# Optimization experiments

Hardware: AMD Instinct MI355X
Metric: run time of the kernel (lower is better)

Reference implementation:

```python
import jax, jax.numpy as jnp
import numpy as np

H, W, D = 160, 160, 16
VOXEL_SIZE = 0.4
VOL_MIN = np.array([-32.0, -32.0, -1.0], dtype=np.float32)
SCALE_MULTIPLIER = 3.0
N_GAUSS = 8192
CHUNK = 64


def setup_inputs() -> dict:
    key = jax.random.key(0)
    k1, k2, k3, k4, k5 = jax.random.split(key, 5)
    vol_min = jnp.asarray(VOL_MIN)
    vol_ext = jnp.array([64.0, 64.0, 6.4], dtype=jnp.float32)
    means3d = jax.random.uniform(k1, (N_GAUSS, 3), jnp.float32) * vol_ext + vol_min
    opacities = jax.random.uniform(k2, (N_GAUSS, 1), jnp.float32)
    # per-axis std devs: 0.2..0.8 m so 3-sigma footprint spans a handful of voxels
    scales = 0.2 + 0.6 * jax.random.uniform(k3, (N_GAUSS, 3), jnp.float32)
    rotations = jax.random.normal(k4, (N_GAUSS, 4), jnp.float32)
    features = jax.random.normal(k5, (N_GAUSS, 32), jnp.float32)
    return {"means3d": means3d, "opacities": opacities, "scales": scales,
            "rotations": rotations, "features": features}


def quat_to_rotmat(q):
    # q: [N,4] wxyz, normalized
    w, x, y, z = q[:, 0], q[:, 1], q[:, 2], q[:, 3]
    R = jnp.stack([
        jnp.stack([1 - 2 * (y * y + z * z), 2 * (x * y - w * z), 2 * (x * z + w * y)], -1),
        jnp.stack([2 * (x * y + w * z), 1 - 2 * (x * x + z * z), 2 * (y * z - w * x)], -1),
        jnp.stack([2 * (x * z - w * y), 2 * (y * z + w * x), 1 - 2 * (x * x + y * y)], -1),
    ], axis=-2)  # [N,3,3]
    return R


def _grid_coords():
    ii, jj, kk = jnp.meshgrid(jnp.arange(H), jnp.arange(W), jnp.arange(D), indexing="ij")
    idx = jnp.stack([ii, jj, kk], axis=-1).astype(jnp.float32)
    return (idx + 0.5) * VOXEL_SIZE + jnp.asarray(VOL_MIN)  # [H,W,D,3] voxel centers


def reference(means3d, opacities, scales, rotations, features):
    x = _grid_coords().reshape(-1, 3)  # [V,3]
    q = rotations / jnp.linalg.norm(rotations, axis=-1, keepdims=True)
    R = quat_to_rotmat(q)
    # covariance = R diag(s^2) R^T
    cov = jnp.einsum("nij,nj,nkj->nik", R, scales * scales, R)
    cov_inv = jnp.linalg.inv(cov)
    sigma = jnp.sqrt(jnp.diagonal(cov, axis1=1, axis2=2))  # [N,3]
    opac = opacities[:, 0]  # [N]
    n = means3d.shape[0]
    nchunks = n // CHUNK

    def chunked(a):
        return a.reshape(nchunks, CHUNK, *a.shape[1:])

    def step(acc, c):
        mu, op, sg, ci, ft = c
        diff = x[:, None, :] - mu[None, :, :]  # [V,CHUNK,3]
        maha = jnp.einsum("vci,cij,vcj->vc", diff, ci, diff)
        # local aggregation cutoff: within scale_multiplier * sigma box around mean
        mask = jnp.all(jnp.abs(diff) <= SCALE_MULTIPLIER * sg[None, :, :], axis=-1)
        w = op[None, :] * jnp.exp(-0.5 * maha) * mask  # [V,CHUNK]
        return acc + w @ ft, None

    acc0 = jnp.zeros((x.shape[0], features.shape[-1]), jnp.float32)
    xs = (chunked(means3d), chunked(opac), chunked(sigma), chunked(cov_inv), chunked(features))
    acc, _ = jax.lax.scan(step, acc0, xs)
    return acc.reshape(H, W, D, features.shape[-1])
```

## Files before the change

### kernel.cpp

```cpp
#include <hip/hip_runtime.h>

#define HH 160
#define WW 160
#define DD 16
#define NG 8192
#define VOXEL 0.4f

#define TTX 20
#define TTY 20
#define TTZ 4
#define NTILES (TTX * TTY * TTZ)
#define CAP 256


__global__ __launch_bounds__(64) void gv_precompute_bin(
    const float* __restrict__ means, const float* __restrict__ opac,
    const float* __restrict__ scales, const float* __restrict__ rots,
    float4* __restrict__ pack, int* __restrict__ tileCnt,
    int* __restrict__ tileList) {
  int g = blockIdx.x * 64 + threadIdx.x;
  if (g >= NG) return;
  float qw = rots[g * 4 + 0], qx = rots[g * 4 + 1];
  float qy = rots[g * 4 + 2], qz = rots[g * 4 + 3];
  float inv = rsqrtf(qw * qw + qx * qx + qy * qy + qz * qz);
  qw *= inv; qx *= inv; qy *= inv; qz *= inv;
  float R[3][3];
  R[0][0] = 1.f - 2.f * (qy * qy + qz * qz);
  R[0][1] = 2.f * (qx * qy - qw * qz);
  R[0][2] = 2.f * (qx * qz + qw * qy);
  R[1][0] = 2.f * (qx * qy + qw * qz);
  R[1][1] = 1.f - 2.f * (qx * qx + qz * qz);
  R[1][2] = 2.f * (qy * qz - qw * qx);
  R[2][0] = 2.f * (qx * qz - qw * qy);
  R[2][1] = 2.f * (qy * qz + qw * qx);
  R[2][2] = 1.f - 2.f * (qx * qx + qy * qy);
  float sx = scales[g * 3 + 0], sy = scales[g * 3 + 1], sz = scales[g * 3 + 2];
  float s2[3] = {sx * sx, sy * sy, sz * sz};
  float is2[3] = {1.f / s2[0], 1.f / s2[1], 1.f / s2[2]};
  float cov00 = 0.f, cov11 = 0.f, cov22 = 0.f;
  float ci00 = 0.f, ci01 = 0.f, ci02 = 0.f, ci11 = 0.f, ci12 = 0.f, ci22 = 0.f;
#pragma unroll
  for (int c = 0; c < 3; c++) {
    cov00 += R[0][c] * R[0][c] * s2[c];
    cov11 += R[1][c] * R[1][c] * s2[c];
    cov22 += R[2][c] * R[2][c] * s2[c];
    ci00 += R[0][c] * R[0][c] * is2[c];
    ci01 += R[0][c] * R[1][c] * is2[c];
    ci02 += R[0][c] * R[2][c] * is2[c];
    ci11 += R[1][c] * R[1][c] * is2[c];
    ci12 += R[1][c] * R[2][c] * is2[c];
    ci22 += R[2][c] * R[2][c] * is2[c];
  }
  float mx = means[g * 3 + 0], my = means[g * 3 + 1], mz = means[g * 3 + 2];
  float bx = 3.f * sqrtf(cov00), by = 3.f * sqrtf(cov11), bz = 3.f * sqrtf(cov22);
  float4* p = pack + (size_t)g * 4;
  p[0] = make_float4(mx, my, mz, opac[g]);
  p[1] = make_float4(bx, by, bz, ci00);
  p[2] = make_float4(ci01, ci02, ci11, ci12);
  p[3] = make_float4(ci22, 0.f, 0.f, 0.f);

  const float eps = 1e-4f;
  int i0 = (int)ceilf((mx - bx + 32.f) * 2.5f - 0.5f - eps);
  int i1 = (int)floorf((mx + bx + 32.f) * 2.5f - 0.5f + eps);
  int j0 = (int)ceilf((my - by + 32.f) * 2.5f - 0.5f - eps);
  int j1 = (int)floorf((my + by + 32.f) * 2.5f - 0.5f + eps);
  int k0 = (int)ceilf((mz - bz + 1.f) * 2.5f - 0.5f - eps);
  int k1 = (int)floorf((mz + bz + 1.f) * 2.5f - 0.5f + eps);
  i0 = max(i0, 0); i1 = min(i1, HH - 1);
  j0 = max(j0, 0); j1 = min(j1, WW - 1);
  k0 = max(k0, 0); k1 = min(k1, DD - 1);
  if (i0 > i1 || j0 > j1 || k0 > k1) return;
  int ti0 = i0 >> 3, ti1 = i1 >> 3;
  int tj0 = j0 >> 3, tj1 = j1 >> 3;
  int tk0 = k0 >> 2, tk1 = k1 >> 2;
  for (int ti = ti0; ti <= ti1; ti++)
    for (int tj = tj0; tj <= tj1; tj++)
      for (int tk = tk0; tk <= tk1; tk++) {
        int t = (ti * TTY + tj) * TTZ + tk;
        int pos = atomicAdd(&tileCnt[t], 1);
        if (pos < CAP) tileList[t * CAP + pos] = g;
      }
}

__global__ __launch_bounds__(256) void gv_voxelize(
    const float4* __restrict__ pack, const float4* __restrict__ feats,
    const int* __restrict__ tileCnt, const int* __restrict__ tileList,
    float4* __restrict__ out) {
  int tid = threadIdx.x;
  int dk = tid & 3, dj = (tid >> 2) & 7, di = tid >> 5;
  int tk = blockIdx.x, tj = blockIdx.y, ti = blockIdx.z;
  int i = ti * 8 + di, j = tj * 8 + dj, k = tk * 4 + dk;

  float px = (i + 0.5f) * VOXEL - 32.f;
  float py = (j + 0.5f) * VOXEL - 32.f;
  float pz = (k + 0.5f) * VOXEL - 1.f;

  int t = (ti * TTY + tj) * TTZ + tk;
  int cnt = min(tileCnt[t], CAP);
  const int* lst = tileList + t * CAP;

  float4 acc[8];
#pragma unroll
  for (int f = 0; f < 8; f++) acc[f] = make_float4(0.f, 0.f, 0.f, 0.f);

#pragma unroll 2
  for (int n = 0; n < cnt; n++) {
    int gg = lst[n];
    const float4* p = pack + (size_t)gg * 4;
    float4 pa = p[0];
    float4 pb = p[1];
    float dx = px - pa.x, dy = py - pa.y, dz = pz - pa.z;
    bool in = (fabsf(dx) <= pb.x) & (fabsf(dy) <= pb.y) & (fabsf(dz) <= pb.z);
    if (__any(in)) {
      float4 pc = p[2];
      float4 pd = p[3];
      float maha = pb.w * dx * dx + pc.z * dy * dy + pd.x * dz * dz +
                   2.f * (pc.x * dx * dy + pc.y * dx * dz + pc.w * dy * dz);
      float w = in ? pa.w * __expf(-0.5f * maha) : 0.f;
      const float4* ft = feats + (size_t)gg * 8;
#pragma unroll
      for (int f = 0; f < 8; f++) {
        float4 fv = ft[f];
        acc[f].x += w * fv.x;
        acc[f].y += w * fv.y;
        acc[f].z += w * fv.z;
        acc[f].w += w * fv.w;
      }
    }
  }

  size_t v = ((size_t)i * WW + j) * DD + k;
  float4* o = out + v * 8;
#pragma unroll
  for (int f = 0; f < 8; f++) o[f] = acc[f];
}

extern "C" void kernel_launch(void* const* d_in, const int* in_sizes, int n_in,
                              void* d_out, int out_size, void* d_ws, size_t ws_size,
                              hipStream_t stream) {
  const float* means  = (const float*)d_in[0];
  const float* opac   = (const float*)d_in[1];
  const float* scales = (const float*)d_in[2];
  const float* rots   = (const float*)d_in[3];
  const float4* feats = (const float4*)d_in[4];

  char* ws = (char*)d_ws;
  float4* pack   = (float4*)ws;
  int* tileCnt   = (int*)(ws + 512 * 1024);
  int* tileList  = (int*)(ws + 520 * 1024);

  hipMemsetAsync(tileCnt, 0, NTILES * sizeof(int), stream);
  gv_precompute_bin<<<NG / 64, 64, 0, stream>>>(means, opac, scales, rots,
                                                pack, tileCnt, tileList);
  dim3 grid(TTZ, TTY, TTX);
  gv_voxelize<<<grid, 256, 0, stream>>>(pack, feats, tileCnt, tileList,
                                        (float4*)d_out);
}
```

Before: 138.2 us.

## Shrink voxel tiles to one wave each and scalarize Gaussian parameter loads

Binning moves from 8x8x4 to 4x4x4 voxel tiles, and each 64-lane wave now owns one tile, so every voxel tests fewer Gaussians that cannot reach it. Each wave loads its tile's index list cooperatively, one index per lane. It then broadcasts each index with shfl plus readfirstlane, which makes the parameter and feature addresses wave-uniform and lets them become scalar loads. The per-Gaussian __any early-out is dropped, and per-tile capacity falls to 128. In exchange there are more binning atomics, a larger tile list, and a risk of silent truncation if a tile ever holds more than 128 Gaussians.

New measurement: 129.4 us. 6.3% less time.

```diff
diff --git a/kernel.cpp b/kernel.cpp
--- a/kernel.cpp
+++ b/kernel.cpp
@@ -6,11 +6,11 @@
 #define NG 8192
 #define VOXEL 0.4f
 
-#define TTX 20
-#define TTY 20
+#define TTX 40
+#define TTY 40
 #define TTZ 4
 #define NTILES (TTX * TTY * TTZ)
-#define CAP 256
+#define CAP 128
 
 
 __global__ __launch_bounds__(64) void gv_precompute_bin(
@@ -70,8 +70,8 @@
   j0 = max(j0, 0); j1 = min(j1, WW - 1);
   k0 = max(k0, 0); k1 = min(k1, DD - 1);
   if (i0 > i1 || j0 > j1 || k0 > k1) return;
-  int ti0 = i0 >> 3, ti1 = i1 >> 3;
-  int tj0 = j0 >> 3, tj1 = j1 >> 3;
+  int ti0 = i0 >> 2, ti1 = i1 >> 2;
+  int tj0 = j0 >> 2, tj1 = j1 >> 2;
   int tk0 = k0 >> 2, tk1 = k1 >> 2;
   for (int ti = ti0; ti <= ti1; ti++)
     for (int tj = tj0; tj <= tj1; tj++)
@@ -82,14 +82,17 @@
       }
 }
 
-__global__ __launch_bounds__(256) void gv_voxelize(
+__global__ __launch_bounds__(128) void gv_voxelize(
     const float4* __restrict__ pack, const float4* __restrict__ feats,
     const int* __restrict__ tileCnt, const int* __restrict__ tileList,
     float4* __restrict__ out) {
   int tid = threadIdx.x;
-  int dk = tid & 3, dj = (tid >> 2) & 7, di = tid >> 5;
-  int tk = blockIdx.x, tj = blockIdx.y, ti = blockIdx.z;
-  int i = ti * 8 + di, j = tj * 8 + dj, k = tk * 4 + dk;
+  int lane = tid & 63;
+  int wv = tid >> 6;
+  int di = (lane >> 4) & 3, dj = (lane >> 2) & 3, dk = lane & 3;
+  int tk = blockIdx.x * 2 + wv;
+  int tj = blockIdx.y, ti = blockIdx.z;
+  int i = ti * 4 + di, j = tj * 4 + dj, k = tk * 4 + dk;
 
   float px = (i + 0.5f) * VOXEL - 32.f;
   float py = (j + 0.5f) * VOXEL - 32.f;
@@ -103,21 +106,25 @@
 #pragma unroll
   for (int f = 0; f < 8; f++) acc[f] = make_float4(0.f, 0.f, 0.f, 0.f);
 
+  for (int base = 0; base < cnt; base += 64) {
+    int m = min(64, cnt - base);
+    int lidx = lst[base + min(lane, m - 1)];
+
 #pragma unroll 2
-  for (int n = 0; n < cnt; n++) {
-    int gg = lst[n];
-    const float4* p = pack + (size_t)gg * 4;
-    float4 pa = p[0];
-    float4 pb = p[1];
-    float dx = px - pa.x, dy = py - pa.y, dz = pz - pa.z;
-    bool in = (fabsf(dx) <= pb.x) & (fabsf(dy) <= pb.y) & (fabsf(dz) <= pb.z);
-    if (__any(in)) {
-      float4 pc = p[2];
-      float4 pd = p[3];
-      float maha = pb.w * dx * dx + pc.z * dy * dy + pd.x * dz * dz +
-                   2.f * (pc.x * dx * dy + pc.y * dx * dz + pc.w * dy * dz);
-      float w = in ? pa.w * __expf(-0.5f * maha) : 0.f;
+    for (int n = 0; n < m; n++) {
+      int gg = __builtin_amdgcn_readfirstlane(__shfl(lidx, n, 64));
+      const float* p = (const float*)(pack + (size_t)gg * 4);
+      float mux = p[0], muy = p[1], muz = p[2], op = p[3];
+      float bbx = p[4], bby = p[5], bbz = p[6], c00 = p[7];
+      float c01 = p[8], c02 = p[9], c11 = p[10], c12 = p[11];
+      float c22 = p[12];
       const float4* ft = feats + (size_t)gg * 8;
+
+      float dx = px - mux, dy = py - muy, dz = pz - muz;
+      bool in = (fabsf(dx) <= bbx) & (fabsf(dy) <= bby) & (fabsf(dz) <= bbz);
+      float maha = c00 * dx * dx + c11 * dy * dy + c22 * dz * dz +
+                   2.f * (c01 * dx * dy + c02 * dx * dz + c12 * dy * dz);
+      float w = in ? op * __expf(-0.5f * maha) : 0.f;
 #pragma unroll
       for (int f = 0; f < 8; f++) {
         float4 fv = ft[f];
@@ -147,12 +154,12 @@
   char* ws = (char*)d_ws;
   float4* pack   = (float4*)ws;
   int* tileCnt   = (int*)(ws + 512 * 1024);
-  int* tileList  = (int*)(ws + 520 * 1024);
+  int* tileList  = (int*)(ws + 544 * 1024);
 
   hipMemsetAsync(tileCnt, 0, NTILES * sizeof(int), stream);
   gv_precompute_bin<<<NG / 64, 64, 0, stream>>>(means, opac, scales, rots,
                                                 pack, tileCnt, tileList);
-  dim3 grid(TTZ, TTY, TTX);
-  gv_voxelize<<<grid, 256, 0, stream>>>(pack, feats, tileCnt, tileList,
+  dim3 grid(2, TTY, TTX);
+  gv_voxelize<<<grid, 128, 0, stream>>>(pack, feats, tileCnt, tileList,
                                         (float4*)d_out);
 }
```
